# Kernel optimization log

Measured on AMD Instinct MI355X. Metric: run time of the kernel, lower is better.

Reference implementation:

```python
import jax, jax.numpy as jnp
import numpy as np

K = 2        # top-k experts
ALPHA = 0.01  # load-balance loss weight
BETA = 0.1    # z-router loss weight

B, T, D, E = 4, 4096, 2048, 64


def setup_inputs() -> dict:
    key = jax.random.key(0)
    kx, kw = jax.random.split(key)
    x = jax.random.normal(kx, (B, T, D), dtype=jnp.float32)
    W = jax.random.normal(kw, (D, E), dtype=jnp.float32) * (1.0 / np.sqrt(D))
    b = jnp.zeros((E,), dtype=jnp.float32)
    return {"x": x, "W": W, "b": b}


def reference(x, W, b):
    # Router logits and softmax: [B, T, E]
    logits = jnp.einsum("btd,de->bte", x, W) + b
    scores = jax.nn.softmax(logits, axis=-1)

    # Top-k selection and renormalized combine weights: [B, T, K]
    topk_vals, topk_idx = jax.lax.top_k(scores, K)
    combine = topk_vals / jnp.sum(topk_vals, axis=-1, keepdims=True)

    # Load-balance loss (Fedus et al. 2022): f_e = fraction of tokens whose
    # max score is expert e; P_e = mean prob mass on expert e.
    is_max = (scores == jnp.max(scores, axis=-1, keepdims=True)).astype(jnp.float32)
    f = jnp.mean(is_max, axis=(0, 1))   # [E]
    P = jnp.mean(scores, axis=(0, 1))   # [E]
    balance_loss = ALPHA * jnp.mean(f * P)

    # Z-router loss; faithfully applied to post-softmax scores as in source.
    lse = jax.nn.logsumexp(scores, axis=-1)  # [B, T]
    z_loss = BETA * jnp.mean(lse ** 2)

    return topk_idx, combine, balance_loss, z_loss
```

## Files before the change

kernel.cpp:

```cpp
#include <hip/hip_runtime.h>
#include <math.h>

#define NTOK 16384
#define DDIM 2048
#define NEXP 64
#define MT   32
#define KCH  64
#define NCH  (DDIM / KCH)

#define ACC_N  129
#define WF_OFF 256
#define VSTRIDE ((size_t)4 * 64 * 64 * 8)

typedef __attribute__((ext_vector_type(8))) short short8_t;
typedef __attribute__((ext_vector_type(4))) float f32x4;

__device__ __forceinline__ unsigned short f2bf(float f) {
    unsigned int u = __float_as_uint(f);
    u += 0x7fffu + ((u >> 16) & 1u);
    return (unsigned short)(u >> 16);
}
__device__ __forceinline__ float bf2f(unsigned short s) {
    return __uint_as_float(((unsigned int)s) << 16);
}

__global__ __launch_bounds__(256) void prep(
    const float* __restrict__ W, float* __restrict__ ws)
{
    const int i = blockIdx.x * 256 + threadIdx.x;
    if (blockIdx.x == 0 && threadIdx.x < ACC_N) ws[threadIdx.x] = 0.0f;
    const int k = i >> 6, e = i & 63;
    const float v = W[i];
    unsigned short h = f2bf(v);
    float r1 = v - bf2f(h);
    unsigned short m = f2bf(r1);
    unsigned short l = f2bf(r1 - bf2f(m));
    unsigned short* wf = (unsigned short*)(ws + WF_OFF);
    const int g = e >> 4, ks = k >> 5;
    const int lane = (((k >> 3) & 3) << 4) | (e & 15);
    const int j = k & 7;
    const size_t base = ((((size_t)g * 64) + ks) * 64 + lane) * 8 + j;
    wf[base] = h;
    wf[VSTRIDE + base] = m;
    wf[2 * VSTRIDE + base] = l;
}

__device__ __forceinline__ void conv_store(
    unsigned short* dh, unsigned short* dm, unsigned short* dl,
    float4 a0, float4 a1)
{
    float xv[8];
    *(float4*)&xv[0] = a0; *(float4*)&xv[4] = a1;
    unsigned short th[8], tm[8], tl[8];
    #pragma unroll
    for (int i = 0; i < 8; ++i) {
        float f = xv[i];
        th[i] = f2bf(f);
        float r = f - bf2f(th[i]);
        tm[i] = f2bf(r);
        tl[i] = f2bf(r - bf2f(tm[i]));
    }
    *(short8_t*)dh = *(short8_t*)&th[0];
    *(short8_t*)dm = *(short8_t*)&tm[0];
    *(short8_t*)dl = *(short8_t*)&tl[0];
}

__global__ __launch_bounds__(256, 4) void gate_fused(
    const float* __restrict__ x, const unsigned short* __restrict__ wf,
    const float* __restrict__ bias, float* __restrict__ out,
    float* __restrict__ acc_g)
{
    __shared__ __align__(16) unsigned short xh[2][MT * KCH];
    __shared__ __align__(16) unsigned short xm_[2][MT * KCH];
    __shared__ __align__(16) unsigned short xl_[2][MT * KCH];
    __shared__ float logits[MT][68];
    __shared__ int   f_loc[NEXP];
    __shared__ float p_loc[NEXP];
    __shared__ float z_loc;

    const int tid  = threadIdx.x;
    const int tok0 = blockIdx.x * MT;
    const int lane = tid & 63;
    const int g    = __builtin_amdgcn_readfirstlane(tid >> 6);

    if (tid < NEXP) { f_loc[tid] = 0; p_loc[tid] = 0.0f; }
    if (tid == 0) z_loc = 0.0f;

    const int srow = tid >> 3;
    const int scg  = tid & 7;
    const float* xs = x + (size_t)(tok0 + srow) * DDIM + scg * 8;
    const int wbase = srow * KCH;
    const int s0 = ((scg ^ (srow & 7))) * 8;

    const int arow16 = lane & 15;
    const int akq    = lane >> 4;
    const int asw    = arow16 & 7;

    f32x4 acc[2][3];
    #pragma unroll
    for (int q = 0; q < 2; ++q)
        #pragma unroll
        for (int ch = 0; ch < 3; ++ch)
            acc[q][ch] = (f32x4){0.f, 0.f, 0.f, 0.f};

    {
        float4 a0 = *(const float4*)(xs + 0);
        float4 a1 = *(const float4*)(xs + 4);
        conv_store(&xh[0][wbase + s0], &xm_[0][wbase + s0],
                   &xl_[0][wbase + s0], a0, a1);
    }
    float4 pv0 = *(const float4*)(xs + KCH + 0);
    float4 pv1 = *(const float4*)(xs + KCH + 4);

    #pragma unroll 1
    for (int c = 0; c < NCH; ++c) {
        __syncthreads();
        const int cb = c & 1, nb = cb ^ 1;

        if (c + 1 < NCH) {
            conv_store(&xh[nb][wbase + s0], &xm_[nb][wbase + s0],
                       &xl_[nb][wbase + s0], pv0, pv1);
            if (c + 2 < NCH) {
                const float* xn = xs + (c + 2) * KCH;
                pv0 = *(const float4*)(xn + 0);
                pv1 = *(const float4*)(xn + 4);
            }
        }

        __builtin_amdgcn_s_setprio(1);
        #pragma unroll
        for (int s = 0; s < 2; ++s) {
            const int ks = c * 2 + s;
            const unsigned short* wb =
                wf + ((((size_t)g * 64) + ks) * 64 + lane) * 8;
            short8_t bh = *(const short8_t*)&wb[0];
            short8_t bm = *(const short8_t*)&wb[VSTRIDE];
            short8_t bl = *(const short8_t*)&wb[2 * VSTRIDE];
            const int slot = (((s * 4 + akq) ^ asw)) * 8;
            #pragma unroll
            for (int q = 0; q < 2; ++q) {
                const int ab = (16 * q + arow16) * KCH + slot;
                short8_t ah = *(const short8_t*)&xh[cb][ab];
                short8_t am = *(const short8_t*)&xm_[cb][ab];
                short8_t al = *(const short8_t*)&xl_[cb][ab];
                acc[q][0] = __builtin_amdgcn_mfma_f32_16x16x32_bf16(ah, bh, acc[q][0], 0, 0, 0);
                acc[q][1] = __builtin_amdgcn_mfma_f32_16x16x32_bf16(ah, bm, acc[q][1], 0, 0, 0);
                acc[q][2] = __builtin_amdgcn_mfma_f32_16x16x32_bf16(am, bm, acc[q][2], 0, 0, 0);
                acc[q][0] = __builtin_amdgcn_mfma_f32_16x16x32_bf16(ah, bl, acc[q][0], 0, 0, 0);
                acc[q][1] = __builtin_amdgcn_mfma_f32_16x16x32_bf16(am, bh, acc[q][1], 0, 0, 0);
                acc[q][2] = __builtin_amdgcn_mfma_f32_16x16x32_bf16(al, bh, acc[q][2], 0, 0, 0);
            }
        }
        __builtin_amdgcn_s_setprio(0);
    }

    #pragma unroll
    for (int q = 0; q < 2; ++q)
        #pragma unroll
        for (int r = 0; r < 4; ++r)
            logits[16 * q + akq * 4 + r][g * 16 + arow16] =
                (acc[q][0][r] + acc[q][1][r]) + acc[q][2][r];
    __syncthreads();

    const int tx  = tid & 15;
    const int tgs = tid >> 4;
    const int e0  = tx * 4;

    float bb[4];
    *(float4*)bb = *(const float4*)&bias[e0];

    float pacc[4] = {0.f, 0.f, 0.f, 0.f};
    float zacc = 0.0f;

    #pragma unroll
    for (int it = 0; it < 2; ++it) {
        const int t  = it * 16 + tgs;
        const int gt = tok0 + t;

        float l[4];
        {
            float4 lv = *(const float4*)&logits[t][e0];
            l[0] = lv.x + bb[0]; l[1] = lv.y + bb[1];
            l[2] = lv.z + bb[2]; l[3] = lv.w + bb[3];
        }

        float v1 = l[0], v2 = -INFINITY;
        int   i1 = e0,   i2 = 0x7fffffff;
        #pragma unroll
        for (int j = 1; j < 4; ++j) {
            float v = l[j]; int e = e0 + j;
            if (v > v1)      { v2 = v1; i2 = i1; v1 = v; i1 = e; }
            else if (v > v2) { v2 = v;  i2 = e; }
        }
        #pragma unroll
        for (int off = 1; off < 16; off <<= 1) {
            float o1 = __shfl_xor(v1, off, 16); int oi1 = __shfl_xor(i1, off, 16);
            float o2 = __shfl_xor(v2, off, 16); int oi2 = __shfl_xor(i2, off, 16);
            if (o1 > v1 || (o1 == v1 && oi1 < i1)) {
                float cs = v1; int ci = i1;
                v1 = o1; i1 = oi1;
                if (cs > o2 || (cs == o2 && ci < oi2)) { v2 = cs; i2 = ci;  }
                else                                   { v2 = o2; i2 = oi2; }
            } else {
                if (o1 > v2 || (o1 == v2 && oi1 < i2)) { v2 = o1; i2 = oi1; }
            }
        }
        const float mx = v1;

        float sden[4], dsum = 0.0f;
        #pragma unroll
        for (int j = 0; j < 4; ++j) { sden[j] = __expf(l[j] - mx); dsum += sden[j]; }
        #pragma unroll
        for (int off = 1; off < 16; off <<= 1) dsum += __shfl_xor(dsum, off, 16);
        const float inv = 1.0f / dsum;

        float zsum = 0.0f;
        #pragma unroll
        for (int j = 0; j < 4; ++j) {
            float pj = sden[j] * inv;
            pacc[j] += pj;
            zsum += __expf(pj);
        }
        #pragma unroll
        for (int off = 1; off < 16; off <<= 1) zsum += __shfl_xor(zsum, off, 16);

        if (tx == 0) {
            const float s2 = __expf(v2 - mx);
            const float ci = 1.0f / (1.0f + s2);
            out[2 * gt]     = (float)i1;
            out[2 * gt + 1] = (float)i2;
            out[2 * NTOK + 2 * gt]     = ci;
            out[2 * NTOK + 2 * gt + 1] = s2 * ci;
            atomicAdd(&f_loc[i1], 1);
            float lse = __logf(zsum);
            zacc += lse * lse;
        }
    }

    #pragma unroll
    for (int off = 1; off < 64; off <<= 1) zacc += __shfl_xor(zacc, off);
    if ((tid & 63) == 0) atomicAdd(&z_loc, zacc);

    #pragma unroll
    for (int j = 0; j < 4; ++j) {
        pacc[j] += __shfl_xor(pacc[j], 16);
        pacc[j] += __shfl_xor(pacc[j], 32);
    }
    if ((tid & 63) < 16) {
        #pragma unroll
        for (int j = 0; j < 4; ++j) atomicAdd(&p_loc[e0 + j], pacc[j]);
    }

    __syncthreads();
    if (tid < NEXP) {
        atomicAdd(&acc_g[64 + tid], p_loc[tid]);
        if (f_loc[tid]) atomicAdd(&acc_g[tid], (float)f_loc[tid]);
    }
    if (tid == 0) atomicAdd(&acc_g[128], z_loc);
}

__global__ void gate_finalize(const float* __restrict__ acc, float* __restrict__ out) {
    int e = threadIdx.x;
    float v = acc[e] * acc[64 + e];
    #pragma unroll
    for (int off = 32; off > 0; off >>= 1) v += __shfl_down(v, off);
    if (e == 0) {
        const float NT = (float)NTOK;
        out[2 * NTOK * 2]     = 0.01f * (v / (float)NEXP) / (NT * NT);
        out[2 * NTOK * 2 + 1] = 0.1f * acc[128] / NT;
    }
}

extern "C" void kernel_launch(void* const* d_in, const int* in_sizes, int n_in,
                              void* d_out, int out_size, void* d_ws, size_t ws_size,
                              hipStream_t stream) {
    const float* x    = (const float*)d_in[0];
    const float* W    = (const float*)d_in[1];
    const float* bias = (const float*)d_in[2];
    float* out = (float*)d_out;
    float* ws  = (float*)d_ws;
    const unsigned short* wfrag = (const unsigned short*)(ws + WF_OFF);

    prep<<<(DDIM * NEXP) / 256, 256, 0, stream>>>(W, ws);
    gate_fused<<<NTOK / MT, 256, 0, stream>>>(x, wfrag, bias, out, ws);
    gate_finalize<<<1, 64, 0, stream>>>(ws, out);
}
```

Baseline: 65.84 us.

## Stage W fragments into LDS via async global_load_lds and halve K chunk

The pre-split bf16 W fragments are now staged into double-buffered LDS with asynchronous global-to-LDS loads, issued one chunk ahead, instead of being read straight from global memory inside the MFMA loop. The K chunk shrinks from 64 to 32, so each iteration runs one MFMA k-step with 4-element x conversion per thread, the XOR swizzle is dropped, and occupancy hint goes from 4 to 3 blocks. The aim is to hide W load latency behind compute. In exchange it doubles the number of barriers, and there is no explicit wait on the async LDS loads before they are consumed.

```diff
diff --git a/kernel.cpp b/kernel.cpp
--- a/kernel.cpp
+++ b/kernel.cpp
@@ -5,7 +5,7 @@
 #define DDIM 2048
 #define NEXP 64
 #define MT   32
-#define KCH  64
+#define KCH  32
 #define NCH  (DDIM / KCH)
 
 #define ACC_N  129
@@ -13,6 +13,7 @@
 #define VSTRIDE ((size_t)4 * 64 * 64 * 8)
 
 typedef __attribute__((ext_vector_type(8))) short short8_t;
+typedef __attribute__((ext_vector_type(4))) short short4_t;
 typedef __attribute__((ext_vector_type(4))) float f32x4;
 
 __device__ __forceinline__ unsigned short f2bf(float f) {
@@ -22,6 +23,12 @@
 }
 __device__ __forceinline__ float bf2f(unsigned short s) {
     return __uint_as_float(((unsigned int)s) << 16);
+}
+
+__device__ __forceinline__ void gload16(const void* g, const void* lds) {
+    __builtin_amdgcn_global_load_lds(
+        (const __attribute__((address_space(1))) unsigned int*)g,
+        (__attribute__((address_space(3))) unsigned int*)lds, 16, 0, 0);
 }
 
 __global__ __launch_bounds__(256) void prep(
@@ -45,34 +52,13 @@
     wf[2 * VSTRIDE + base] = l;
 }
 
-__device__ __forceinline__ void conv_store(
-    unsigned short* dh, unsigned short* dm, unsigned short* dl,
-    float4 a0, float4 a1)
-{
-    float xv[8];
-    *(float4*)&xv[0] = a0; *(float4*)&xv[4] = a1;
-    unsigned short th[8], tm[8], tl[8];
-    #pragma unroll
-    for (int i = 0; i < 8; ++i) {
-        float f = xv[i];
-        th[i] = f2bf(f);
-        float r = f - bf2f(th[i]);
-        tm[i] = f2bf(r);
-        tl[i] = f2bf(r - bf2f(tm[i]));
-    }
-    *(short8_t*)dh = *(short8_t*)&th[0];
-    *(short8_t*)dm = *(short8_t*)&tm[0];
-    *(short8_t*)dl = *(short8_t*)&tl[0];
-}
-
-__global__ __launch_bounds__(256, 4) void gate_fused(
+__global__ __launch_bounds__(256, 3) void gate_fused(
     const float* __restrict__ x, const unsigned short* __restrict__ wf,
     const float* __restrict__ bias, float* __restrict__ out,
     float* __restrict__ acc_g)
 {
-    __shared__ __align__(16) unsigned short xh[2][MT * KCH];
-    __shared__ __align__(16) unsigned short xm_[2][MT * KCH];
-    __shared__ __align__(16) unsigned short xl_[2][MT * KCH];
+    __shared__ __align__(16) unsigned short xa[2][3][MT * KCH];
+    __shared__ __align__(16) unsigned short bl_[2][3][256 * 8];
     __shared__ float logits[MT][68];
     __shared__ int   f_loc[NEXP];
     __shared__ float p_loc[NEXP];
@@ -87,14 +73,16 @@
     if (tid == 0) z_loc = 0.0f;
 
     const int srow = tid >> 3;
-    const int scg  = tid & 7;
-    const float* xs = x + (size_t)(tok0 + srow) * DDIM + scg * 8;
-    const int wbase = srow * KCH;
-    const int s0 = ((scg ^ (srow & 7))) * 8;
+    const int cg   = tid & 7;
+    const float* xs = x + (size_t)(tok0 + srow) * DDIM + cg * 4;
+    const int abase_w = srow * KCH + cg * 4;
+
+    const int g2 = tid >> 6, lane2 = tid & 63;
+    const unsigned short* wsrc =
+        wf + (((size_t)g2 * 64) * 64 + lane2) * 8;
 
     const int arow16 = lane & 15;
     const int akq    = lane >> 4;
-    const int asw    = arow16 & 7;
 
     f32x4 acc[2][3];
     #pragma unroll
@@ -104,13 +92,26 @@
             acc[q][ch] = (f32x4){0.f, 0.f, 0.f, 0.f};
 
     {
-        float4 a0 = *(const float4*)(xs + 0);
-        float4 a1 = *(const float4*)(xs + 4);
-        conv_store(&xh[0][wbase + s0], &xm_[0][wbase + s0],
-                   &xl_[0][wbase + s0], a0, a1);
-    }
-    float4 pv0 = *(const float4*)(xs + KCH + 0);
-    float4 pv1 = *(const float4*)(xs + KCH + 4);
+        float4 a0 = *(const float4*)xs;
+        float xv[4];
+        *(float4*)xv = a0;
+        unsigned short th[4], tm[4], tl[4];
+        #pragma unroll
+        for (int i = 0; i < 4; ++i) {
+            float f = xv[i];
+            th[i] = f2bf(f);
+            float r = f - bf2f(th[i]);
+            tm[i] = f2bf(r);
+            tl[i] = f2bf(r - bf2f(tm[i]));
+        }
+        *(short4_t*)&xa[0][0][abase_w] = *(short4_t*)&th[0];
+        *(short4_t*)&xa[0][1][abase_w] = *(short4_t*)&tm[0];
+        *(short4_t*)&xa[0][2][abase_w] = *(short4_t*)&tl[0];
+        #pragma unroll
+        for (int v = 0; v < 3; ++v)
+            gload16(wsrc + (size_t)v * VSTRIDE, &bl_[0][v][tid * 8]);
+    }
+    float4 pv = *(const float4*)(xs + KCH);
 
     #pragma unroll 1
     for (int c = 0; c < NCH; ++c) {
@@ -118,38 +119,45 @@
         const int cb = c & 1, nb = cb ^ 1;
 
         if (c + 1 < NCH) {
-            conv_store(&xh[nb][wbase + s0], &xm_[nb][wbase + s0],
-                       &xl_[nb][wbase + s0], pv0, pv1);
-            if (c + 2 < NCH) {
-                const float* xn = xs + (c + 2) * KCH;
-                pv0 = *(const float4*)(xn + 0);
-                pv1 = *(const float4*)(xn + 4);
+            const unsigned short* wsn = wsrc + (size_t)(c + 1) * 64 * 8;
+            #pragma unroll
+            for (int v = 0; v < 3; ++v)
+                gload16(wsn + (size_t)v * VSTRIDE, &bl_[nb][v][tid * 8]);
+            float xv[4];
+            *(float4*)xv = pv;
+            unsigned short th[4], tm[4], tl[4];
+            #pragma unroll
+            for (int i = 0; i < 4; ++i) {
+                float f = xv[i];
+                th[i] = f2bf(f);
+                float r = f - bf2f(th[i]);
+                tm[i] = f2bf(r);
+                tl[i] = f2bf(r - bf2f(tm[i]));
             }
+            *(short4_t*)&xa[nb][0][abase_w] = *(short4_t*)&th[0];
+            *(short4_t*)&xa[nb][1][abase_w] = *(short4_t*)&tm[0];
+            *(short4_t*)&xa[nb][2][abase_w] = *(short4_t*)&tl[0];
+            if (c + 2 < NCH)
+                pv = *(const float4*)(xs + (c + 2) * KCH);
         }
 
         __builtin_amdgcn_s_setprio(1);
-        #pragma unroll
-        for (int s = 0; s < 2; ++s) {
-            const int ks = c * 2 + s;
-            const unsigned short* wb =
-                wf + ((((size_t)g * 64) + ks) * 64 + lane) * 8;
-            short8_t bh = *(const short8_t*)&wb[0];
-            short8_t bm = *(const short8_t*)&wb[VSTRIDE];
-            short8_t bl = *(const short8_t*)&wb[2 * VSTRIDE];
-            const int slot = (((s * 4 + akq) ^ asw)) * 8;
-            #pragma unroll
-            for (int q = 0; q < 2; ++q) {
-                const int ab = (16 * q + arow16) * KCH + slot;
-                short8_t ah = *(const short8_t*)&xh[cb][ab];
-                short8_t am = *(const short8_t*)&xm_[cb][ab];
-                short8_t al = *(const short8_t*)&xl_[cb][ab];
-                acc[q][0] = __builtin_amdgcn_mfma_f32_16x16x32_bf16(ah, bh, acc[q][0], 0, 0, 0);
-                acc[q][1] = __builtin_amdgcn_mfma_f32_16x16x32_bf16(ah, bm, acc[q][1], 0, 0, 0);
-                acc[q][2] = __builtin_amdgcn_mfma_f32_16x16x32_bf16(am, bm, acc[q][2], 0, 0, 0);
-                acc[q][0] = __builtin_amdgcn_mfma_f32_16x16x32_bf16(ah, bl, acc[q][0], 0, 0, 0);
-                acc[q][1] = __builtin_amdgcn_mfma_f32_16x16x32_bf16(am, bh, acc[q][1], 0, 0, 0);
-                acc[q][2] = __builtin_amdgcn_mfma_f32_16x16x32_bf16(al, bh, acc[q][2], 0, 0, 0);
-            }
+        const int bb_ = (g * 64 + lane) * 8;
+        short8_t bh = *(const short8_t*)&bl_[cb][0][bb_];
+        short8_t bm = *(const short8_t*)&bl_[cb][1][bb_];
+        short8_t blv = *(const short8_t*)&bl_[cb][2][bb_];
+        #pragma unroll
+        for (int q = 0; q < 2; ++q) {
+            const int ab = (16 * q + arow16) * KCH + akq * 8;
+            short8_t ah = *(const short8_t*)&xa[cb][0][ab];
+            short8_t am = *(const short8_t*)&xa[cb][1][ab];
+            short8_t al = *(const short8_t*)&xa[cb][2][ab];
+            acc[q][0] = __builtin_amdgcn_mfma_f32_16x16x32_bf16(ah, bh,  acc[q][0], 0, 0, 0);
+            acc[q][1] = __builtin_amdgcn_mfma_f32_16x16x32_bf16(ah, bm,  acc[q][1], 0, 0, 0);
+            acc[q][2] = __builtin_amdgcn_mfma_f32_16x16x32_bf16(am, bm,  acc[q][2], 0, 0, 0);
+            acc[q][0] = __builtin_amdgcn_mfma_f32_16x16x32_bf16(ah, blv, acc[q][0], 0, 0, 0);
+            acc[q][1] = __builtin_amdgcn_mfma_f32_16x16x32_bf16(am, bh,  acc[q][1], 0, 0, 0);
+            acc[q][2] = __builtin_amdgcn_mfma_f32_16x16x32_bf16(al, bh,  acc[q][2], 0, 0, 0);
         }
         __builtin_amdgcn_s_setprio(0);
     }
@@ -166,8 +174,8 @@
     const int tgs = tid >> 4;
     const int e0  = tx * 4;
 
-    float bb[4];
-    *(float4*)bb = *(const float4*)&bias[e0];
+    float bbv[4];
+    *(float4*)bbv = *(const float4*)&bias[e0];
 
     float pacc[4] = {0.f, 0.f, 0.f, 0.f};
     float zacc = 0.0f;
@@ -180,8 +188,8 @@
         float l[4];
         {
             float4 lv = *(const float4*)&logits[t][e0];
-            l[0] = lv.x + bb[0]; l[1] = lv.y + bb[1];
-            l[2] = lv.z + bb[2]; l[3] = lv.w + bb[3];
+            l[0] = lv.x + bbv[0]; l[1] = lv.y + bbv[1];
+            l[2] = lv.z + bbv[2]; l[3] = lv.w + bbv[3];
         }
 
         float v1 = l[0], v2 = -INFINITY;
```

Measured after the change: 75.20 us. 1.14x slower.
